# Performance work log

Measured on AMD Instinct MI355X. Metric: run time of the kernel, lower is better.

## Reference

```python
import jax, jax.numpy as jnp
import numpy as np

N_HEADS = 16
N_UNITS = 1024
D_K = N_UNITS // N_HEADS
B, S = 2, 2048


def setup_inputs() -> dict:
    key = jax.random.key(0)
    ks = jax.random.split(key, 12)
    bound = 1.0 / np.sqrt(N_UNITS)
    u = lambda k, shape: jax.random.uniform(k, shape, jnp.float32, -bound, bound)
    inp = {
        'query': jax.random.normal(ks[0], (B, S, N_UNITS), jnp.float32),
        'key_': jax.random.normal(ks[1], (B, S, N_UNITS), jnp.float32),
        'value': jax.random.normal(ks[2], (B, S, N_UNITS), jnp.float32),
        'mask': jnp.broadcast_to(jnp.tril(jnp.ones((S, S), jnp.int32)), (B, S, S)),
        'Wq': u(ks[3], (N_UNITS, N_UNITS)), 'bq': u(ks[4], (N_UNITS,)),
        'Wk': u(ks[5], (N_UNITS, N_UNITS)), 'bk': u(ks[6], (N_UNITS,)),
        'Wv': u(ks[7], (N_UNITS, N_UNITS)), 'bv': u(ks[8], (N_UNITS,)),
        'Wo': u(ks[9], (N_UNITS, N_UNITS)), 'bo': u(ks[10], (N_UNITS,)),
    }
    return inp


def _split_heads(x):
    # [B,S,U] -> [B,H,S,Dk]
    b, s, _ = x.shape
    return x.reshape(b, s, N_HEADS, D_K).transpose(0, 2, 1, 3)


def reference(query, key_, value, mask, Wq, bq, Wk, bk, Wv, bv, Wo, bo):
    q = _split_heads(query @ Wq.T + bq)
    k = _split_heads(key_ @ Wk.T + bk)
    v = _split_heads(value @ Wv.T + bv)
    scores = jnp.einsum('bhqd,bhkd->bhqk', q, k) / jnp.sqrt(jnp.float32(D_K))
    scores = jnp.where(mask[:, None, :, :] == 0, jnp.float32(-1e10), scores)
    attn = jax.nn.softmax(scores, axis=-1)  # dropout omitted (eval / p=0)
    A = jnp.einsum('bhqk,bhkd->bhqd', attn, v)
    A = A.transpose(0, 2, 1, 3).reshape(query.shape[0], -1, N_UNITS)
    return A @ Wo.T + bo
```

## Files before the change

### kernel.cpp

```cpp
#include <hip/hip_runtime.h>
#include <hip/hip_bf16.h>

#define U     1024
#define SLEN  2048
#define HEADS 16
#define DK    64
#define MTOT  4096
#define MU    (MTOT * U)
#define UU    (U * U)

#define QSCALE2 0.18033688f

typedef unsigned short u16;
typedef short bf16x8 __attribute__((ext_vector_type(8)));
typedef u16 u16x4 __attribute__((ext_vector_type(4)));
typedef float f32x4 __attribute__((ext_vector_type(4)));

__device__ __forceinline__ u16 f2bf(float x) {
  union { float f; unsigned int u; } v; v.f = x;
  unsigned int r = v.u + 0x7fffu + ((v.u >> 16) & 1u);
  return (u16)(r >> 16);
}
__device__ __forceinline__ u16 f2bf_rz(float x) {
  return (u16)(__builtin_bit_cast(unsigned int, x) >> 16);
}

#if __has_builtin(__builtin_amdgcn_exp2f)
__device__ __forceinline__ float exp2_fast(float x) { return __builtin_amdgcn_exp2f(x); }
#else
__device__ __forceinline__ float exp2_fast(float x) { return __expf(x * 0.6931472f); }
#endif

__device__ __forceinline__ void async16(const u16* g, u16* lds) {
  __builtin_amdgcn_global_load_lds((const __attribute__((address_space(1))) void*)g,
                                   (__attribute__((address_space(3))) void*)lds,
                                   16, 0, 0);
}

#define DPP_F(x, ctrl) __builtin_bit_cast(float, \
    __builtin_amdgcn_update_dpp(0, __builtin_bit_cast(int, (x)), (ctrl), 0xF, 0xF, true))

__device__ __forceinline__ float rsum16(float x) {
  x += DPP_F(x, 0xB1);
  x += DPP_F(x, 0x4E);
  x += DPP_F(x, 0x141);
  x += DPP_F(x, 0x140);
  return x;
}

__global__ __launch_bounds__(256) void convert_kernel(
    const float* __restrict__ q, const float* __restrict__ k, const float* __restrict__ v,
    const float* __restrict__ wq, const float* __restrict__ wk,
    const float* __restrict__ wv, const float* __restrict__ wo,
    u16* __restrict__ cq, u16* __restrict__ ck, u16* __restrict__ cv,
    u16* __restrict__ cwq, u16* __restrict__ cwk, u16* __restrict__ cwv,
    u16* __restrict__ cwo) {
  const int t = blockIdx.y;
  const float* src = (t == 0) ? q : (t == 1) ? k : (t == 2) ? v
                   : (t == 3) ? wq : (t == 4) ? wk : (t == 5) ? wv : wo;
  u16* dst = (t == 0) ? cq : (t == 1) ? ck : (t == 2) ? cv
           : (t == 3) ? cwq : (t == 4) ? cwk : (t == 5) ? cwv : cwo;
  const int n4 = ((t < 3) ? MU : UU) >> 2;
  const int stride = gridDim.x * blockDim.x;
  for (int i = blockIdx.x * blockDim.x + threadIdx.x; i < n4; i += stride) {
    float4 f = ((const float4*)src)[i];
    u16x4 o = {f2bf(f.x), f2bf(f.y), f2bf(f.z), f2bf(f.w)};
    ((u16x4*)dst)[i] = o;
  }
}

__device__ __forceinline__ void stage_tile(const u16* __restrict__ src, int kt,
                                           u16* lds, int tid) {
#pragma unroll
  for (int c = 0; c < 2; ++c) {
    int f = c * 256 + tid;
    int row = f >> 2;
    int qs = f & 3;
    int q = qs ^ ((row >> 1) & 3);
    const u16* g = src + (size_t)row * U + kt + q * 8;
    u16* l = lds + (size_t)(f & ~63) * 8;
    async16(g, l);
  }
}

__device__ __forceinline__ bf16x8 read_frag(const u16* lds, int lrow, int quad) {
  int qs = quad ^ ((lrow >> 1) & 3);
  return *(const bf16x8*)(lds + (size_t)(lrow * 4 + qs) * 8);
}

__device__ __forceinline__ void gemm128(const u16* __restrict__ X,
                                        const u16* __restrict__ W,
                                        int m0, int n0, int tid,
                                        u16* lds_a, u16* lds_b,
                                        f32x4 acc[4][4]) {
  const int l = tid & 63, w = tid >> 6;
  const int quad = l >> 4, l15 = l & 15;
  const int wm = w & 1, wn = w >> 1;
  const u16* Xb = X + (size_t)m0 * U;
  const u16* Wb = W + (size_t)n0 * U;
  for (int kt = 0; kt < U; kt += 32) {
    stage_tile(Xb, kt, lds_a, tid);
    stage_tile(Wb, kt, lds_b, tid);
    __syncthreads();
    bf16x8 af[4], bfm[4];
#pragma unroll
    for (int i = 0; i < 4; ++i) af[i] = read_frag(lds_a, wm * 64 + i * 16 + l15, quad);
#pragma unroll
    for (int t = 0; t < 4; ++t) bfm[t] = read_frag(lds_b, wn * 64 + t * 16 + l15, quad);
#pragma unroll
    for (int i = 0; i < 4; ++i)
#pragma unroll
      for (int t = 0; t < 4; ++t)
        acc[i][t] = __builtin_amdgcn_mfma_f32_16x16x32_bf16(af[i], bfm[t], acc[i][t], 0, 0, 0);
    __syncthreads();
  }
}

__global__ __launch_bounds__(256) void qkv_gemm(
    const u16* __restrict__ q_in, const u16* __restrict__ k_in, const u16* __restrict__ v_in,
    const u16* __restrict__ Wq, const u16* __restrict__ Wk, const u16* __restrict__ Wv,
    const float* __restrict__ bq, const float* __restrict__ bk, const float* __restrict__ bv,
    u16* __restrict__ q_ws, u16* __restrict__ k_ws, u16* __restrict__ v_ws) {
  __shared__ __align__(16) u16 lds_a[4096];
  __shared__ __align__(16) u16 lds_b[4096];
  const int z = blockIdx.z;
  const u16* X = (z == 0) ? q_in : (z == 1) ? k_in : v_in;
  const u16* W = (z == 0) ? Wq : (z == 1) ? Wk : Wv;
  const float* bias = (z == 0) ? bq : (z == 1) ? bk : bv;
  const int m0 = blockIdx.y * 128, n0 = blockIdx.x * 128;
  const int tid = threadIdx.x;
  f32x4 acc[4][4];
#pragma unroll
  for (int i = 0; i < 4; ++i)
#pragma unroll
    for (int t = 0; t < 4; ++t) acc[i][t] = (f32x4){0.f, 0.f, 0.f, 0.f};
  gemm128(X, W, m0, n0, tid, lds_a, lds_b, acc);

  const int l = tid & 63, w = tid >> 6;
  const int quad = l >> 4, l15 = l & 15;
  const int wm = w & 1, wn = w >> 1;
  const float osc = (z == 0) ? QSCALE2 : 1.0f;
#pragma unroll
  for (int t = 0; t < 4; ++t) {
    const int n = n0 + wn * 64 + t * 16 + l15;
    const float bb = bias[n];
    const int h = n >> 6, d = n & 63;
#pragma unroll
    for (int i = 0; i < 4; ++i) {
#pragma unroll
      for (int r = 0; r < 4; ++r) {
        const int m = m0 + wm * 64 + i * 16 + quad * 4 + r;
        const int b = m >> 11, s = m & (SLEN - 1);
        const int bh = b * HEADS + h;
        const u16 ov = f2bf((acc[i][t][r] + bb) * osc);
        if (z == 0)      q_ws[((size_t)bh * SLEN + s) * DK + d] = ov;
        else if (z == 1) k_ws[((size_t)bh * SLEN + s) * DK + d] = ov;
        else             v_ws[((size_t)bh * DK + d) * SLEN + s] = ov;
      }
    }
  }
}

__global__ __launch_bounds__(256, 4) void flash_attn(const u16* __restrict__ q_ws,
                                                     const u16* __restrict__ k_ws,
                                                     const u16* __restrict__ v_ws,
                                                     u16* __restrict__ a_ws) {
  __shared__ __align__(16) u16 kbuf[2][4096];
  __shared__ __align__(16) u16 vbuf[2][4096];
  __shared__ __align__(16) u16 p_lds[4][16][72];
  const int id = blockIdx.x;
  const int bh = id & 31;
  const int qblk = 31 - (id >> 5);
  const int tid = threadIdx.x;
  const int w = tid >> 6, l = tid & 63;
  const int quad = l >> 4, l15 = l & 15;
  const int qrow = qblk * 64 + w * 16;
  const int jn = qblk;

  const u16* qb = q_ws + (size_t)bh * SLEN * DK;
  const u16* kb = k_ws + (size_t)bh * SLEN * DK;
  const u16* vb = v_ws + (size_t)bh * DK * SLEN;

  bf16x8 aq0 = *(const bf16x8*)(qb + (size_t)(qrow + l15) * DK + quad * 8);
  bf16x8 aq1 = *(const bf16x8*)(qb + (size_t)(qrow + l15) * DK + 32 + quad * 8);

  f32x4 o[4];
  float l_run[4];
#pragma unroll
  for (int t = 0; t < 4; ++t) o[t] = (f32x4){0.f, 0.f, 0.f, 0.f};
#pragma unroll
  for (int r = 0; r < 4; ++r) l_run[r] = 0.f;

  auto stage = [&](int j0, int b) {
#pragma unroll
    for (int c = 0; c < 2; ++c) {
      const int f = c * 256 + tid;
      const int row = f >> 3, qs = f & 7;
      const int q = qs ^ (row & 7);
      u16* kdst = kbuf[b] + (size_t)(f & ~63) * 8;
      u16* vdst = vbuf[b] + (size_t)(f & ~63) * 8;
      async16(kb + (size_t)(j0 + row) * DK + q * 8, kdst);
      async16(vb + (size_t)row * SLEN + j0 + q * 8, vdst);
    }
  };

  stage(0, 0);
  __syncthreads();

  for (int jt = 0; jt <= jn; ++jt) {
    const int buf = jt & 1;
    if (jt < jn) stage((jt + 1) * 64, buf ^ 1);
    const int j0 = jt * 64;
    const int swz = l15 & 7;

    float sv[4][4];
#pragma unroll
    for (int t = 0; t < 4; ++t) {
      const u16* krow = kbuf[buf] + (size_t)(t * 16 + l15) * 64;
      bf16x8 kf0 = *(const bf16x8*)(krow + ((quad ^ swz) * 8));
      bf16x8 kf1 = *(const bf16x8*)(krow + (((quad + 4) ^ swz) * 8));
      f32x4 acc = (f32x4){0.f, 0.f, 0.f, 0.f};
      acc = __builtin_amdgcn_mfma_f32_16x16x32_bf16(aq0, kf0, acc, 0, 0, 0);
      acc = __builtin_amdgcn_mfma_f32_16x16x32_bf16(aq1, kf1, acc, 0, 0, 0);
#pragma unroll
      for (int r = 0; r < 4; ++r) sv[t][r] = acc[r];
    }
    if (jt == jn) {
#pragma unroll
      for (int t = 0; t < 4; ++t) {
        const int col = j0 + t * 16 + l15;
#pragma unroll
        for (int r = 0; r < 4; ++r)
          if (col > qrow + quad * 4 + r) sv[t][r] = -1e30f;
      }
    }
#pragma unroll
    for (int t = 0; t < 4; ++t) {
#pragma unroll
      for (int r = 0; r < 4; ++r) {
        const float p = exp2_fast(sv[t][r]);
        l_run[r] += p;
        p_lds[w][quad * 4 + r][t * 16 + l15] = f2bf_rz(p);
      }
    }
    bf16x8 pa0 = *(const bf16x8*)&p_lds[w][l15][quad * 8];
    bf16x8 pa1 = *(const bf16x8*)&p_lds[w][l15][32 + quad * 8];
#pragma unroll
    for (int t = 0; t < 4; ++t) {
      const u16* vrow = vbuf[buf] + (size_t)(t * 16 + l15) * 64;
      bf16x8 vf0 = *(const bf16x8*)(vrow + ((quad ^ swz) * 8));
      bf16x8 vf1 = *(const bf16x8*)(vrow + (((quad + 4) ^ swz) * 8));
      o[t] = __builtin_amdgcn_mfma_f32_16x16x32_bf16(pa0, vf0, o[t], 0, 0, 0);
      o[t] = __builtin_amdgcn_mfma_f32_16x16x32_bf16(pa1, vf1, o[t], 0, 0, 0);
    }
    __syncthreads();
  }
  const int b = bh >> 4, h = bh & 15;
  float inv[4];
#pragma unroll
  for (int r = 0; r < 4; ++r) inv[r] = 1.f / rsum16(l_run[r]);
#pragma unroll
  for (int r = 0; r < 4; ++r) {
    const int s = qrow + quad * 4 + r;
    u16* orow = a_ws + ((size_t)b * SLEN + s) * U + h * DK;
#pragma unroll
    for (int t = 0; t < 4; ++t)
      orow[t * 16 + l15] = f2bf(o[t][r] * inv[r]);
  }
}

__global__ __launch_bounds__(256) void oproj_gemm(const u16* __restrict__ A,
                                                  const u16* __restrict__ Wo,
                                                  const float* __restrict__ bo,
                                                  float* __restrict__ out) {
  __shared__ __align__(16) u16 lds_a[4096];
  __shared__ __align__(16) u16 lds_b[4096];
  const int m0 = blockIdx.y * 128, n0 = blockIdx.x * 128;
  const int tid = threadIdx.x;
  f32x4 acc[4][4];
#pragma unroll
  for (int i = 0; i < 4; ++i)
#pragma unroll
    for (int t = 0; t < 4; ++t) acc[i][t] = (f32x4){0.f, 0.f, 0.f, 0.f};
  gemm128(A, Wo, m0, n0, tid, lds_a, lds_b, acc);

  const int l = tid & 63, w = tid >> 6;
  const int quad = l >> 4, l15 = l & 15;
  const int wm = w & 1, wn = w >> 1;
#pragma unroll
  for (int t = 0; t < 4; ++t) {
    const int n = n0 + wn * 64 + t * 16 + l15;
    const float bb = bo[n];
#pragma unroll
    for (int i = 0; i < 4; ++i) {
#pragma unroll
      for (int r = 0; r < 4; ++r) {
        const int m = m0 + wm * 64 + i * 16 + quad * 4 + r;
        out[(size_t)m * U + n] = acc[i][t][r] + bb;
      }
    }
  }
}

extern "C" void kernel_launch(void* const* d_in, const int* in_sizes, int n_in,
                              void* d_out, int out_size, void* d_ws, size_t ws_size,
                              hipStream_t stream) {
  (void)in_sizes; (void)n_in; (void)out_size; (void)ws_size;
  const float* query = (const float*)d_in[0];
  const float* key_  = (const float*)d_in[1];
  const float* value = (const float*)d_in[2];
  const float* Wq = (const float*)d_in[4];
  const float* bq = (const float*)d_in[5];
  const float* Wk = (const float*)d_in[6];
  const float* bk = (const float*)d_in[7];
  const float* Wv = (const float*)d_in[8];
  const float* bv = (const float*)d_in[9];
  const float* Wo = (const float*)d_in[10];
  const float* bo = (const float*)d_in[11];

  u16* ws = (u16*)d_ws;
  u16* cq  = ws;
  u16* ck  = cq + MU;
  u16* cv  = ck + MU;
  u16* cwq = cv + MU;
  u16* cwk = cwq + UU;
  u16* cwv = cwk + UU;
  u16* cwo = cwv + UU;
  u16* q_ws = cwo + UU;
  u16* k_ws = q_ws + MU;
  u16* v_ws = k_ws + MU;
  u16* a_ws = v_ws + MU;
  float* out = (float*)d_out;

  convert_kernel<<<dim3(512, 7), 256, 0, stream>>>(query, key_, value, Wq, Wk, Wv, Wo,
                                                   cq, ck, cv, cwq, cwk, cwv, cwo);
  qkv_gemm<<<dim3(8, 32, 3), 256, 0, stream>>>(cq, ck, cv, cwq, cwk, cwv,
                                               bq, bk, bv, q_ws, k_ws, v_ws);
  flash_attn<<<dim3(1024), 256, 0, stream>>>(q_ws, k_ws, v_ws, a_ws);
  oproj_gemm<<<dim3(8, 32), 256, 0, stream>>>(a_ws, cwo, bo, out);
}
```

Measured before the change: 241.9 us.

## Triple-buffer GEMM LDS tiles with async prefetch and remap blocks across XCDs

The shared 128x128 GEMM loop now uses three LDS buffers. It prefetches the next K-tile with async loads while computing the current one, and replaces the two __syncthreads per iteration with one barrier plus a partial vmcnt wait. Block indices are also remapped so that tiles sharing rows land on the same XCD, to improve L2 reuse. This adds more LDS per block, which may reduce occupancy, and the remap assumes a fixed 8x32 grid shape.

```diff
diff --git a/kernel.cpp b/kernel.cpp
--- a/kernel.cpp
+++ b/kernel.cpp
@@ -91,29 +91,56 @@
 __device__ __forceinline__ void gemm128(const u16* __restrict__ X,
                                         const u16* __restrict__ W,
                                         int m0, int n0, int tid,
-                                        u16* lds_a, u16* lds_b,
+                                        u16* lds,
                                         f32x4 acc[4][4]) {
   const int l = tid & 63, w = tid >> 6;
   const int quad = l >> 4, l15 = l & 15;
   const int wm = w & 1, wn = w >> 1;
   const u16* Xb = X + (size_t)m0 * U;
   const u16* Wb = W + (size_t)n0 * U;
+
+  stage_tile(Xb, 0, lds, tid);
+  stage_tile(Wb, 0, lds + 4096, tid);
+
+  int bufsel = 0;
   for (int kt = 0; kt < U; kt += 32) {
-    stage_tile(Xb, kt, lds_a, tid);
-    stage_tile(Wb, kt, lds_b, tid);
-    __syncthreads();
+    const int nxt = (bufsel == 2) ? 0 : bufsel + 1;
+    if (kt + 32 < U) {
+      stage_tile(Xb, kt + 32, lds + nxt * 8192, tid);
+      stage_tile(Wb, kt + 32, lds + nxt * 8192 + 4096, tid);
+      __builtin_amdgcn_sched_barrier(0);
+      asm volatile("s_waitcnt vmcnt(4)" ::: "memory");
+    } else {
+      __builtin_amdgcn_sched_barrier(0);
+      asm volatile("s_waitcnt vmcnt(0)" ::: "memory");
+    }
+    __builtin_amdgcn_sched_barrier(0);
+    __builtin_amdgcn_s_barrier();
+    __builtin_amdgcn_sched_barrier(0);
+
+    const u16* la = lds + bufsel * 8192;
+    const u16* lb = la + 4096;
     bf16x8 af[4], bfm[4];
 #pragma unroll
-    for (int i = 0; i < 4; ++i) af[i] = read_frag(lds_a, wm * 64 + i * 16 + l15, quad);
-#pragma unroll
-    for (int t = 0; t < 4; ++t) bfm[t] = read_frag(lds_b, wn * 64 + t * 16 + l15, quad);
+    for (int i = 0; i < 4; ++i) af[i] = read_frag(la, wm * 64 + i * 16 + l15, quad);
+#pragma unroll
+    for (int t = 0; t < 4; ++t) bfm[t] = read_frag(lb, wn * 64 + t * 16 + l15, quad);
 #pragma unroll
     for (int i = 0; i < 4; ++i)
 #pragma unroll
       for (int t = 0; t < 4; ++t)
         acc[i][t] = __builtin_amdgcn_mfma_f32_16x16x32_bf16(af[i], bfm[t], acc[i][t], 0, 0, 0);
-    __syncthreads();
-  }
+    bufsel = nxt;
+  }
+}
+
+__device__ __forceinline__ void xcd_remap(int* m0, int* n0) {
+  const int id = blockIdx.x + (blockIdx.y << 3);
+  const int k = id & 7, j = id >> 3;
+  const int xp = j >> 2;
+  const int yp = (k << 2) | (j & 3);
+  *m0 = yp * 128;
+  *n0 = xp * 128;
 }
 
 __global__ __launch_bounds__(256) void qkv_gemm(
@@ -121,20 +148,20 @@
     const u16* __restrict__ Wq, const u16* __restrict__ Wk, const u16* __restrict__ Wv,
     const float* __restrict__ bq, const float* __restrict__ bk, const float* __restrict__ bv,
     u16* __restrict__ q_ws, u16* __restrict__ k_ws, u16* __restrict__ v_ws) {
-  __shared__ __align__(16) u16 lds_a[4096];
-  __shared__ __align__(16) u16 lds_b[4096];
+  __shared__ __align__(16) u16 lds3[3 * 8192];
   const int z = blockIdx.z;
   const u16* X = (z == 0) ? q_in : (z == 1) ? k_in : v_in;
   const u16* W = (z == 0) ? Wq : (z == 1) ? Wk : Wv;
   const float* bias = (z == 0) ? bq : (z == 1) ? bk : bv;
-  const int m0 = blockIdx.y * 128, n0 = blockIdx.x * 128;
+  int m0, n0;
+  xcd_remap(&m0, &n0);
   const int tid = threadIdx.x;
   f32x4 acc[4][4];
 #pragma unroll
   for (int i = 0; i < 4; ++i)
 #pragma unroll
     for (int t = 0; t < 4; ++t) acc[i][t] = (f32x4){0.f, 0.f, 0.f, 0.f};
-  gemm128(X, W, m0, n0, tid, lds_a, lds_b, acc);
+  gemm128(X, W, m0, n0, tid, lds3, acc);
 
   const int l = tid & 63, w = tid >> 6;
   const int quad = l >> 4, l15 = l & 15;
@@ -273,16 +300,16 @@
                                                   const u16* __restrict__ Wo,
                                                   const float* __restrict__ bo,
                                                   float* __restrict__ out) {
-  __shared__ __align__(16) u16 lds_a[4096];
-  __shared__ __align__(16) u16 lds_b[4096];
-  const int m0 = blockIdx.y * 128, n0 = blockIdx.x * 128;
+  __shared__ __align__(16) u16 lds3[3 * 8192];
+  int m0, n0;
+  xcd_remap(&m0, &n0);
   const int tid = threadIdx.x;
   f32x4 acc[4][4];
 #pragma unroll
   for (int i = 0; i < 4; ++i)
 #pragma unroll
     for (int t = 0; t < 4; ++t) acc[i][t] = (f32x4){0.f, 0.f, 0.f, 0.f};
-  gemm128(A, Wo, m0, n0, tid, lds_a, lds_b, acc);
+  gemm128(A, Wo, m0, n0, tid, lds3, acc);
 
   const int l = tid & 63, w = tid >> 6;
   const int quad = l >> 4, l15 = l & 15;
```

Result: faster. 230.7 us (-4.6%).
